# Optimization experiments

Measured on AMD Instinct MI355X. Metric: run time of the kernel, lower is better.

The kernel has to match this reference:

```python
import jax, jax.numpy as jnp
import numpy as np
import math

N_HEAD = 16
N_HEAD_KV = 4
WINDOW = 1024
SINK = 4
ROPE_BASE = 10000.0


def _rope(x):
    # x: [B, H, T, D]; rotate-half RoPE
    B, H, T, D = x.shape
    inv_freq = 1.0 / (ROPE_BASE ** (jnp.arange(0, D, 2, dtype=jnp.float32) / D))  # [D/2]
    ang = jnp.arange(T, dtype=jnp.float32)[:, None] * inv_freq[None, :]  # [T, D/2]
    cos = jnp.concatenate([jnp.cos(ang), jnp.cos(ang)], axis=-1)  # [T, D]
    sin = jnp.concatenate([jnp.sin(ang), jnp.sin(ang)], axis=-1)
    x1, x2 = x[..., : D // 2], x[..., D // 2 :]
    rot = jnp.concatenate([-x2, x1], axis=-1)
    return x * cos[None, None] + rot * sin[None, None]


def setup_inputs() -> dict:
    key = jax.random.key(0)
    ks = jax.random.split(key, 6)
    B, T, C = 2, 2048, 2048
    D = C // N_HEAD
    x = jax.random.normal(ks[0], (B, T, C), dtype=jnp.float32)
    s = 0.02
    Wq = jax.random.normal(ks[1], (C, C), dtype=jnp.float32) * s
    Wk = jax.random.normal(ks[2], (C, N_HEAD_KV * D), dtype=jnp.float32) * s
    Wv = jax.random.normal(ks[3], (C, N_HEAD_KV * D), dtype=jnp.float32) * s
    Wo = jax.random.normal(ks[4], (C, C), dtype=jnp.float32) * s
    seq_lengths = jax.random.randint(ks[5], (B,), T // 2, T + 1, dtype=jnp.int32)
    return {"x": x, "Wq": Wq, "Wk": Wk, "Wv": Wv, "Wo": Wo, "seq_lengths": seq_lengths}


def reference(x, Wq, Wk, Wv, Wo, seq_lengths):
    B, T, C = x.shape
    H, Hkv = N_HEAD, N_HEAD_KV
    D = C // H
    scale = 1.0 / math.sqrt(D)

    q = (x @ Wq).reshape(B, T, H, D).transpose(0, 2, 1, 3)      # [B,H,T,D]
    k = (x @ Wk).reshape(B, T, Hkv, D).transpose(0, 2, 1, 3)    # [B,Hkv,T,D]
    v = (x @ Wv).reshape(B, T, Hkv, D).transpose(0, 2, 1, 3)
    # GQA: repeat kv heads (matches torch repeat_interleave on head dim)
    k = jnp.repeat(k, H // Hkv, axis=1)
    v = jnp.repeat(v, H // Hkv, axis=1)

    q = _rope(q)
    k = _rope(k)

    scores = jnp.einsum('bhqd,bhkd->bhqk', q, k) * scale  # [B,H,T,T]

    qi = jnp.arange(T)[:, None]
    ki = jnp.arange(T)[None, :]
    # causal & (in sliding window | attention sink)
    base = (qi >= ki) & (((qi - ki) <= WINDOW) | (ki < SINK))  # [T,T]
    valid = jnp.arange(T)[None, :] < seq_lengths[:, None]      # [B,T]
    mask = base[None, None] & valid[:, None, :, None] & valid[:, None, None, :]

    scores = jnp.where(mask, scores, -1e30)
    attn = jax.nn.softmax(scores, axis=-1)
    y = jnp.einsum('bhqk,bhkd->bhqd', attn, v)
    # flex_attention returns 0 for fully-masked (padded) query rows
    y = y * valid[:, None, :, None]

    y = y.transpose(0, 2, 1, 3).reshape(B, T, C)
    return y @ Wo
```

## Files before the change

### kernel.cpp

```cpp
#include <hip/hip_runtime.h>
#include <stdint.h>

#define BATCH 2
#define TSEQ  2048
#define CDIM  2048
#define NHEAD 16
#define NKV   4
#define HDIM  128
#define KVDIM 512
#define WIN   1024
#define SINKN 4
#define QT    64
#define QKVN  3072

typedef unsigned short u16;
typedef __attribute__((ext_vector_type(8))) short bf16x8;
typedef __attribute__((ext_vector_type(4))) float f32x4;
typedef __attribute__((address_space(3))) uint32_t as3_u32;
typedef const __attribute__((address_space(1))) uint32_t as1_u32;

__device__ __forceinline__ float bf2f(u16 u) {
  union { uint32_t i; float f; } w; w.i = ((uint32_t)u) << 16; return w.f;
}
__device__ __forceinline__ u16 f2bf(float f) {
  union { uint32_t i; float f; } w; w.f = f;
  return (u16)((w.i + 0x7fffu + ((w.i >> 16) & 1u)) >> 16);
}
__device__ __forceinline__ void gl2lds16(const u16* g, u16* l) {
  __builtin_amdgcn_global_load_lds((as1_u32*)g, (as3_u32*)l, 16, 0, 0);
}

__global__ __launch_bounds__(256)
void detect_kernel(const uint32_t* __restrict__ x, uint32_t* __restrict__ flag) {
  __shared__ int red[4];
  const int tid = threadIdx.x;
  int c = 0;
  for (int i = tid; i < 1024; i += 256) {
    uint32_t e = (x[i] >> 7) & 0xFFu;
    c += (e >= 100u && e <= 135u) ? 1 : 0;
  }
#pragma unroll
  for (int off = 32; off; off >>= 1) c += __shfl_xor(c, off, 64);
  if ((tid & 63) == 0) red[tid >> 6] = c;
  __syncthreads();
  if (tid == 0) flag[0] = ((red[0] + red[1] + red[2] + red[3]) > 512) ? 1u : 0u;
}

__global__ __launch_bounds__(256)
void convert4_kernel(const void* __restrict__ src, u16* __restrict__ dst,
                     int n4, const uint32_t* __restrict__ flag) {
  const int i = blockIdx.x * 256 + threadIdx.x;
  if (i >= n4) return;
  if (flag[0]) {
    ((uint2*)dst)[i] = ((const uint2*)src)[i];
  } else {
    float4 f = ((const float4*)src)[i];
    ushort4 o = { f2bf(f.x), f2bf(f.y), f2bf(f.z), f2bf(f.w) };
    ((ushort4*)dst)[i] = o;
  }
}

__global__ __launch_bounds__(256)
void transpose_w(const void* __restrict__ src, u16* __restrict__ dst,
                 int K, int N, const uint32_t* __restrict__ flag) {
  __shared__ u16 t[32][33];
  const int n0 = blockIdx.x * 32, k0 = blockIdx.y * 32;
  const int tx = threadIdx.x & 31, ty = threadIdx.x >> 5;
  const uint32_t f = flag[0];
#pragma unroll
  for (int i = 0; i < 4; ++i) {
    const int kk = k0 + ty + i * 8;
    u16 val = f ? ((const u16*)src)[(size_t)kk * N + n0 + tx]
                : f2bf(((const float*)src)[(size_t)kk * N + n0 + tx]);
    t[ty + i * 8][tx] = val;
  }
  __syncthreads();
#pragma unroll
  for (int i = 0; i < 4; ++i)
    dst[(size_t)(n0 + ty + i * 8) * K + k0 + tx] = t[tx][ty + i * 8];
}

__global__ __launch_bounds__(256)
void transpose_v(const u16* __restrict__ qkv, u16* __restrict__ vt) {
  __shared__ u16 t[32][33];
  const int tok0 = blockIdx.x * 32;
  const int d0 = blockIdx.y * 32;
  const int bh = blockIdx.z;
  const int b = bh >> 2, kvh = bh & 3;
  const int tx = threadIdx.x & 31, ty = threadIdx.x >> 5;
  const u16* src = qkv + ((size_t)(b * TSEQ + tok0)) * QKVN + 2560 + (kvh << 7) + d0;
#pragma unroll
  for (int i = 0; i < 4; ++i)
    t[ty + i * 8][tx] = src[(size_t)(ty + i * 8) * QKVN + tx];
  __syncthreads();
  u16* dst = vt + ((size_t)(bh * 128 + d0)) * TSEQ + tok0;
#pragma unroll
  for (int i = 0; i < 4; ++i)
    dst[(size_t)(ty + i * 8) * TSEQ + tx] = t[tx][ty + i * 8];
}

#define BAR() asm volatile("s_barrier" ::: "memory")

__device__ __forceinline__ void stage_half(const u16* g, int K, u16* lds,
                                           int w, int lrow, int lc16) {
  gl2lds16(g + (size_t)(w * 8 + lrow) * K + (lc16 << 3), lds + (w << 9));
  gl2lds16(g + (size_t)(64 + w * 8 + lrow) * K + (lc16 << 3), lds + ((8 + w) << 9));
}

__global__ __launch_bounds__(512, 2)
void gemm256(const u16* __restrict__ A, const u16* __restrict__ BT,
             void* __restrict__ C, int M, int N, int K,
             const uint32_t* __restrict__ flagp, const int* __restrict__ seq) {
  __shared__ u16 As[2 * 256 * 64];
  __shared__ u16 Bs[2 * 256 * 64];

  const int tid = threadIdx.x;
  const int w = tid >> 6, lane = tid & 63;
  const int quad = lane >> 4, lm = lane & 15, l8 = lane & 7;
  const int wm = w >> 2, wn = w & 3;
  const int lrow = lane >> 3;
  const int lc16 = (lane & 7) ^ lrow;

  const int gx = gridDim.x;
  const int nwg = gx * gridDim.y;
  int lin = blockIdx.y * gx + blockIdx.x;
  if ((nwg & 7) == 0) lin = (lin & 7) * (nwg >> 3) + (lin >> 3);
  const int m0 = (lin / gx) << 8;
  const int n0 = (lin % gx) << 8;

  if (seq) {
    const int t0 = m0 & (TSEQ - 1);
    if (t0 >= seq[m0 >> 11]) {
      const uint32_t fmz = flagp ? flagp[0] : 1u;
      if (fmz == 0) {
        float4 z = {0.f, 0.f, 0.f, 0.f};
        float* Cp = (float*)C;
        for (int i = tid; i < 256 * 64; i += 512) {
          const int r = i >> 6, c4 = (i & 63) << 2;
          *(float4*)(Cp + (size_t)(m0 + r) * N + n0 + c4) = z;
        }
      } else {
        uint4 z = {0u, 0u, 0u, 0u};
        u16* Cp = (u16*)C;
        for (int i = tid; i < 256 * 32; i += 512) {
          const int r = i >> 5, c8 = (i & 31) << 3;
          *(uint4*)(Cp + (size_t)(m0 + r) * N + n0 + c8) = z;
        }
      }
      return;
    }
  }

  const u16* Agm = A + (size_t)m0 * K;
  const u16* Bgm = BT + (size_t)n0 * K;
  const int NT = K >> 6;

  f32x4 acc[8][4];
#pragma unroll
  for (int i = 0; i < 8; ++i)
#pragma unroll
    for (int j = 0; j < 4; ++j) acc[i][j] = (f32x4){0.f, 0.f, 0.f, 0.f};

  stage_half(Bgm,                     K, Bs,             w, lrow, lc16);
  stage_half(Agm,                     K, As,             w, lrow, lc16);
  stage_half(Bgm + (size_t)128 * K,   K, Bs + 128 * 64,  w, lrow, lc16);
  stage_half(Agm + (size_t)128 * K,   K, As + 128 * 64,  w, lrow, lc16);
  stage_half(Bgm + 64,                K, Bs + 16384,     w, lrow, lc16);
  stage_half(Agm + 64,                K, As + 16384,     w, lrow, lc16);
  asm volatile("s_waitcnt vmcnt(4)" ::: "memory");
  BAR();

  bf16x8 a[4][2], b0[2][2], b1[2][2];

#define LDA_(mh)                                                              \
  _Pragma("unroll") for (int mi = 0; mi < 4; ++mi)                            \
  _Pragma("unroll") for (int ks = 0; ks < 2; ++ks)                            \
    a[mi][ks] = *(const bf16x8*)(Ab + ((wm * 128 + (mh) * 64 + mi * 16 + lm) << 6) + \
                                 (((ks * 4 + quad) ^ l8) << 3));
#define LDB_(dst, nh)                                                         \
  _Pragma("unroll") for (int ni = 0; ni < 2; ++ni)                            \
  _Pragma("unroll") for (int ks = 0; ks < 2; ++ks)                            \
    dst[ni][ks] = *(const bf16x8*)(Bb + ((wn * 64 + (nh) * 32 + ni * 16 + lm) << 6) + \
                                   (((ks * 4 + quad) ^ l8) << 3));
#define MFMA8(mh, nh, bb)                                                     \
  __builtin_amdgcn_s_setprio(1);                                              \
  _Pragma("unroll") for (int mi = 0; mi < 4; ++mi)                            \
  _Pragma("unroll") for (int ni = 0; ni < 2; ++ni)                            \
  _Pragma("unroll") for (int ks = 0; ks < 2; ++ks)                            \
    acc[(mh) * 4 + mi][(nh) * 2 + ni] = __builtin_amdgcn_mfma_f32_16x16x32_bf16( \
        a[mi][ks], bb[ni][ks], acc[(mh) * 4 + mi][(nh) * 2 + ni], 0, 0, 0);   \
  __builtin_amdgcn_s_setprio(0);

  for (int t = 0; t < NT; ++t) {
    const int p = t & 1;
    const u16* Ab = As + p * 16384;
    const u16* Bb = Bs + p * 16384;
    u16* An = (u16*)As + (p ^ 1) * 16384;
    u16* Bn = (u16*)Bs + (p ^ 1) * 16384;
    u16* Ac = (u16*)As + p * 16384;
    u16* Bc = (u16*)Bs + p * 16384;
    const size_t kc1 = (size_t)(t + 1) << 6;
    const size_t kc2 = (size_t)(t + 2) << 6;

    LDA_(0); LDB_(b0, 0);
    if (t + 1 < NT) stage_half(Bgm + (size_t)128 * K + kc1, K, Bn + 128 * 64, w, lrow, lc16);
    BAR();
    MFMA8(0, 0, b0);
    BAR();
    LDB_(b1, 1);
    if (t + 1 < NT) stage_half(Agm + (size_t)128 * K + kc1, K, An + 128 * 64, w, lrow, lc16);
    BAR();
    MFMA8(0, 1, b1);
    BAR();
    LDA_(1);
    if (t + 2 < NT) stage_half(Bgm + kc2, K, Bc, w, lrow, lc16);
    BAR();
    MFMA8(1, 1, b1);
    BAR();
    if (t + 2 < NT) stage_half(Agm + kc2, K, Ac, w, lrow, lc16);
    BAR();
    MFMA8(1, 0, b0);
    if (t >= NT - 2) { asm volatile("s_waitcnt vmcnt(0)" ::: "memory"); }
    else             { asm volatile("s_waitcnt vmcnt(4)" ::: "memory"); }
    BAR();
  }
#undef LDA_
#undef LDB_
#undef MFMA8

  const uint32_t fm = flagp ? flagp[0] : 1u;
#pragma unroll
  for (int mi = 0; mi < 8; ++mi)
#pragma unroll
    for (int ni = 0; ni < 4; ++ni)
#pragma unroll
      for (int r = 0; r < 4; ++r) {
        const int row = m0 + wm * 128 + mi * 16 + quad * 4 + r;
        const int col = n0 + wn * 64 + ni * 16 + lm;
        const float val = acc[mi][ni][r];
        if (fm == 0) ((float*)C)[(size_t)row * N + col] = val;
        else         ((u16*)C)[(size_t)row * N + col] = f2bf(val);
      }
}

__global__ __launch_bounds__(256)
void rope_kernel(u16* __restrict__ qkv) {
  const int QP = BATCH * TSEQ * NHEAD * 64;
  const int KP = BATCH * TSEQ * NKV * 64;
  int idx = blockIdx.x * 256 + threadIdx.x;
  u16* p;
  int i, t;
  if (idx < QP) {
    i = idx & 63;
    int hh = (idx >> 6) & (NHEAD - 1);
    int row = idx >> 10;
    t = row & (TSEQ - 1);
    p = qkv + (size_t)row * QKVN + (hh << 7);
  } else {
    int j = idx - QP;
    if (j >= KP) return;
    i = j & 63;
    int hh = (j >> 6) & (NKV - 1);
    int row = j >> 8;
    t = row & (TSEQ - 1);
    p = qkv + (size_t)row * QKVN + 2048 + (hh << 7);
  }
  float x1 = bf2f(p[i]), x2 = bf2f(p[i + 64]);
  float freq = exp2f((float)i * (-2.0f / 128.0f) * 13.287712379549449f);
  float ang = (float)t * freq;
  float c = cosf(ang), s = sinf(ang);
  p[i]      = f2bf(x1 * c - x2 * s);
  p[i + 64] = f2bf(x2 * c + x1 * s);
}

__global__ __launch_bounds__(256, 3)
void attn_mfma(const u16* __restrict__ qkv, const u16* __restrict__ vt,
               u16* __restrict__ y, const int* __restrict__ seq_lengths) {
  const int bid = blockIdx.x;
  const int q0 = (31 - (bid & 31)) * QT;
  const int h  = (bid >> 5) & (NHEAD - 1);
  const int b  = bid >> 9;
  const int tid = threadIdx.x;
  const int w = tid >> 6;
  const int lane = tid & 63;
  const int quad = lane >> 4;
  const int lm = lane & 15;
  const int L = seq_lengths[b];
  const int kvh = h >> 2;
  const int kvoff = kvh << 7;
  const size_t bT = (size_t)b * TSEQ;

  if (q0 >= L) {
    const uint4 z = {0u, 0u, 0u, 0u};
    for (int i = tid; i < 64 * 256; i += 256) {
      const int r = i >> 8, c8 = (i & 255) << 3;
      *(uint4*)(y + ((bT + q0 + r) << 11) + c8) = z;
    }
    return;
  }

  __shared__ u16 Ks[32 * 136];
  __shared__ u16 Vt[144 * 40];
  __shared__ u16 Ps[4 * 16 * 42];

  const int qbase = q0 + w * 16;

  bf16x8 qf[4];
  {
    const u16* qrow = qkv + (bT + qbase + lm) * QKVN + (h << 7);
#pragma unroll
    for (int c = 0; c < 4; ++c)
      qf[c] = *(const bf16x8*)(qrow + c * 32 + quad * 8);
  }

  for (int i = tid; i < 16 * 40; i += 256)
    Vt[128 * 40 + i] = (i < 40) ? (u16)0x3F80 : (u16)0;

  const int s0k = q0 - WIN > 0 ? q0 - WIN : 0;
  const int sink_extra = (s0k > 0) ? 1 : 0;
  const int niter = ((q0 + QT - s0k) >> 5) + sink_extra;

  f32x4 Oacc[9];
#pragma unroll
  for (int nt = 0; nt < 9; ++nt) Oacc[nt] = (f32x4){0.f, 0.f, 0.f, 0.f};

  const float cexp = 0.127517634f;
  const int trow = tid >> 4;
  const int tc8 = (tid & 15) << 3;
  const int vd = tid >> 2;
  const int vkg = (tid & 3) << 3;
  u16* Pw = Ps + w * 672;

  const u16* kp0 = qkv + (bT + trow) * QKVN + 2048 + kvoff + tc8;
  const u16* kp1 = kp0 + (size_t)16 * QKVN;
  const u16* vp0 = vt + ((size_t)(b * NKV + kvh) << 18) + (size_t)vd * TSEQ + vkg;
  const u16* vp1 = vp0 + (size_t)64 * TSEQ;

  uint4 kr0, kr1, vr0, vr1;
#define LOAD_CHUNK(kb)                                        \
  do {                                                        \
    kr0 = *(const uint4*)(kp0 + (size_t)(kb) * QKVN);         \
    kr1 = *(const uint4*)(kp1 + (size_t)(kb) * QKVN);         \
    vr0 = *(const uint4*)(vp0 + (kb));                        \
    vr1 = *(const uint4*)(vp1 + (kb));                        \
  } while (0)

  int kb_cur = sink_extra ? 0 : s0k;
  int kb_next = sink_extra ? s0k : s0k + 32;
  LOAD_CHUNK(kb_cur);

  for (int it = 0; it < niter; ++it) {
    __syncthreads();
    *(uint4*)(Ks + trow * 136 + tc8)        = kr0;
    *(uint4*)(Ks + (16 + trow) * 136 + tc8) = kr1;
    *(uint4*)(Vt + vd * 40 + vkg)           = vr0;
    *(uint4*)(Vt + (vd + 64) * 40 + vkg)    = vr1;
    if (it + 1 < niter) LOAD_CHUNK(kb_next);
    __syncthreads();

    f32x4 sc0 = {0.f, 0.f, 0.f, 0.f}, sc1 = {0.f, 0.f, 0.f, 0.f};
    __builtin_amdgcn_s_setprio(1);
#pragma unroll
    for (int c = 0; c < 4; ++c) {
      bf16x8 kf = *(const bf16x8*)(Ks + lm * 136 + c * 32 + quad * 8);
      sc0 = __builtin_amdgcn_mfma_f32_16x16x32_bf16(qf[c], kf, sc0, 0, 0, 0);
    }
#pragma unroll
    for (int c = 0; c < 4; ++c) {
      bf16x8 kf = *(const bf16x8*)(Ks + (16 + lm) * 136 + c * 32 + quad * 8);
      sc1 = __builtin_amdgcn_mfma_f32_16x16x32_bf16(qf[c], kf, sc1, 0, 0, 0);
    }
    __builtin_amdgcn_s_setprio(0);

    const int key0 = kb_cur + lm;
    const int key1 = key0 + 16;
#pragma unroll
    for (int r = 0; r < 4; ++r) {
      const int qrow = qbase + quad * 4 + r;
      const bool ok0 = (key0 <= qrow) && ((qrow - key0 <= WIN) || (key0 < SINKN));
      const bool ok1 = (key1 <= qrow) && ((qrow - key1 <= WIN) || (key1 < SINKN));
      const float p0 = ok0 ? exp2f(sc0[r] * cexp) : 0.f;
      const float p1 = ok1 ? exp2f(sc1[r] * cexp) : 0.f;
      const int row = quad * 4 + r;
      Pw[row * 42 + lm]      = f2bf(p0);
      Pw[row * 42 + 16 + lm] = f2bf(p1);
    }
    bf16x8 pf = *(const bf16x8*)(Pw + lm * 42 + quad * 8);
    __builtin_amdgcn_s_setprio(1);
#pragma unroll
    for (int nt = 0; nt < 9; ++nt) {
      bf16x8 vf = *(const bf16x8*)(Vt + (nt * 16 + lm) * 40 + quad * 8);
      Oacc[nt] = __builtin_amdgcn_mfma_f32_16x16x32_bf16(pf, vf, Oacc[nt], 0, 0, 0);
    }
    __builtin_amdgcn_s_setprio(0);
    kb_cur = kb_next;
    kb_next += 32;
  }
#undef LOAD_CHUNK

  float invl[4];
#pragma unroll
  for (int r = 0; r < 4; ++r) {
    const float l = __shfl(Oacc[8][r], lane & 48, 64);
    invl[r] = 1.0f / l;
  }
#pragma unroll
  for (int nt = 0; nt < 8; ++nt)
#pragma unroll
    for (int r = 0; r < 4; ++r) {
      const int qrow = qbase + quad * 4 + r;
      const float val = (qrow < L) ? Oacc[nt][r] * invl[r] : 0.f;
      y[((bT + qrow) << 11) + (h << 7) + nt * 16 + lm] = f2bf(val);
    }
}

extern "C" void kernel_launch(void* const* d_in, const int* in_sizes, int n_in,
                              void* d_out, int out_size, void* d_ws, size_t ws_size,
                              hipStream_t stream) {
  const int M = BATCH * TSEQ;
  const int NX  = M * CDIM;

  uint32_t* flag = (uint32_t*)d_ws;
  u16* base = (u16*)((char*)d_ws + 16);
  u16* qkvb = base;
  u16* yb   = qkvb + (size_t)M * QKVN;
  u16* xb   = yb  + (size_t)NX;
  u16* wqT  = xb  + (size_t)NX;
  u16* wkvT = wqT + (size_t)CDIM * CDIM;
  u16* woT  = wkvT + (size_t)1024 * CDIM;
  u16* vtb  = woT + (size_t)CDIM * CDIM;

  const int* seq = (const int*)d_in[5];

  detect_kernel<<<1, 256, 0, stream>>>((const uint32_t*)d_in[0], flag);
  convert4_kernel<<<(NX / 4 + 255) / 256, 256, 0, stream>>>(d_in[0], xb, NX / 4, flag);
  transpose_w<<<dim3(CDIM / 32, CDIM / 32), 256, 0, stream>>>(d_in[1], wqT, CDIM, CDIM, flag);
  transpose_w<<<dim3(KVDIM / 32, CDIM / 32), 256, 0, stream>>>(d_in[2], wkvT, CDIM, KVDIM, flag);
  transpose_w<<<dim3(KVDIM / 32, CDIM / 32), 256, 0, stream>>>(d_in[3], wkvT + (size_t)KVDIM * CDIM, CDIM, KVDIM, flag);
  transpose_w<<<dim3(CDIM / 32, CDIM / 32), 256, 0, stream>>>(d_in[4], woT, CDIM, CDIM, flag);

  gemm256<<<dim3(QKVN / 256, M / 256), 512, 0, stream>>>(xb, wqT, qkvb, M, QKVN, CDIM, nullptr, seq);
  const int rope_threads = BATCH * TSEQ * (NHEAD + NKV) * 64;
  rope_kernel<<<rope_threads / 256, 256, 0, stream>>>(qkvb);
  transpose_v<<<dim3(TSEQ / 32, HDIM / 32, BATCH * NKV), 256, 0, stream>>>(qkvb, vtb);
  attn_mfma<<<BATCH * NHEAD * (TSEQ / QT), 256, 0, stream>>>(qkvb, vtb, yb, seq);
  gemm256<<<dim3(CDIM / 256, M / 256), 512, 0, stream>>>(yb, woT, d_out, M, CDIM, CDIM, flag, seq);
}
```

Baseline: 364.4 us.

## Make each attention block a single wave processing all four query row tiles

The attention kernel now launches 64-thread blocks. Each block is one wavefront that computes all four 16-row query tiles of a 64-row tile against each shared K/V chunk. This removes the __syncthreads barriers and reuses the K fragments loaded from LDS across the four row tiles. Block order is changed so the heaviest query tiles of every batch/head are scheduled first, and fully padded tiles now zero only their own head's columns instead of the full row. In exchange, each wave holds far more live registers (accumulators for four row tiles plus eight prefetch registers each for K and V), and the total wave count drops by four. That risks spills and much weaker latency hiding.

```diff
diff --git a/kernel.cpp b/kernel.cpp
--- a/kernel.cpp
+++ b/kernel.cpp
@@ -273,16 +273,16 @@
   p[i + 64] = f2bf(x2 * c + x1 * s);
 }
 
-__global__ __launch_bounds__(256, 3)
+__global__ __launch_bounds__(64, 1)
 void attn_mfma(const u16* __restrict__ qkv, const u16* __restrict__ vt,
                u16* __restrict__ y, const int* __restrict__ seq_lengths) {
   const int bid = blockIdx.x;
-  const int q0 = (31 - (bid & 31)) * QT;
-  const int h  = (bid >> 5) & (NHEAD - 1);
-  const int b  = bid >> 9;
-  const int tid = threadIdx.x;
-  const int w = tid >> 6;
-  const int lane = tid & 63;
+  const int tile = 31 - (bid >> 5);
+  const int q0 = tile * QT;
+  const int bh = bid & 31;
+  const int h  = bh & (NHEAD - 1);
+  const int b  = bh >> 4;
+  const int lane = threadIdx.x & 63;
   const int quad = lane >> 4;
   const int lm = lane & 15;
   const int L = seq_lengths[b];
@@ -292,57 +292,50 @@
 
   if (q0 >= L) {
     const uint4 z = {0u, 0u, 0u, 0u};
-    for (int i = tid; i < 64 * 256; i += 256) {
-      const int r = i >> 8, c8 = (i & 255) << 3;
-      *(uint4*)(y + ((bT + q0 + r) << 11) + c8) = z;
+    for (int i = lane; i < 64 * 16; i += 64) {
+      const int r = i >> 4, c8 = (i & 15) << 3;
+      *(uint4*)(y + ((bT + q0 + r) << 11) + (h << 7) + c8) = z;
     }
     return;
   }
 
   __shared__ u16 Ks[32 * 136];
   __shared__ u16 Vt[144 * 40];
-  __shared__ u16 Ps[4 * 16 * 42];
-
-  const int qbase = q0 + w * 16;
-
-  bf16x8 qf[4];
-  {
-    const u16* qrow = qkv + (bT + qbase + lm) * QKVN + (h << 7);
+  __shared__ u16 Pw[16 * 42];
+
+  bf16x8 qf[4][4];
+#pragma unroll
+  for (int rt = 0; rt < 4; ++rt) {
+    const u16* qrow = qkv + (bT + q0 + rt * 16 + lm) * QKVN + (h << 7);
 #pragma unroll
     for (int c = 0; c < 4; ++c)
-      qf[c] = *(const bf16x8*)(qrow + c * 32 + quad * 8);
-  }
-
-  for (int i = tid; i < 16 * 40; i += 256)
+      qf[rt][c] = *(const bf16x8*)(qrow + c * 32 + quad * 8);
+  }
+
+  for (int i = lane; i < 16 * 40; i += 64)
     Vt[128 * 40 + i] = (i < 40) ? (u16)0x3F80 : (u16)0;
 
   const int s0k = q0 - WIN > 0 ? q0 - WIN : 0;
   const int sink_extra = (s0k > 0) ? 1 : 0;
   const int niter = ((q0 + QT - s0k) >> 5) + sink_extra;
 
-  f32x4 Oacc[9];
-#pragma unroll
-  for (int nt = 0; nt < 9; ++nt) Oacc[nt] = (f32x4){0.f, 0.f, 0.f, 0.f};
+  f32x4 Oacc[4][9];
+#pragma unroll
+  for (int rt = 0; rt < 4; ++rt)
+#pragma unroll
+    for (int nt = 0; nt < 9; ++nt) Oacc[rt][nt] = (f32x4){0.f, 0.f, 0.f, 0.f};
 
   const float cexp = 0.127517634f;
-  const int trow = tid >> 4;
-  const int tc8 = (tid & 15) << 3;
-  const int vd = tid >> 2;
-  const int vkg = (tid & 3) << 3;
-  u16* Pw = Ps + w * 672;
-
-  const u16* kp0 = qkv + (bT + trow) * QKVN + 2048 + kvoff + tc8;
-  const u16* kp1 = kp0 + (size_t)16 * QKVN;
-  const u16* vp0 = vt + ((size_t)(b * NKV + kvh) << 18) + (size_t)vd * TSEQ + vkg;
-  const u16* vp1 = vp0 + (size_t)64 * TSEQ;
-
-  uint4 kr0, kr1, vr0, vr1;
-#define LOAD_CHUNK(kb)                                        \
-  do {                                                        \
-    kr0 = *(const uint4*)(kp0 + (size_t)(kb) * QKVN);         \
-    kr1 = *(const uint4*)(kp1 + (size_t)(kb) * QKVN);         \
-    vr0 = *(const uint4*)(vp0 + (kb));                        \
-    vr1 = *(const uint4*)(vp1 + (kb));                        \
+  const u16* kp = qkv + (bT + (lane >> 4)) * QKVN + 2048 + kvoff + ((lane & 15) << 3);
+  const u16* vp = vt + ((size_t)(b * NKV + kvh) << 18) + (size_t)(lane >> 2) * TSEQ + ((lane & 3) << 3);
+
+  uint4 kr[8], vr[8];
+#define LOAD_CHUNK(kb)                                                      \
+  do {                                                                      \
+    _Pragma("unroll") for (int j = 0; j < 8; ++j) {                         \
+      kr[j] = *(const uint4*)(kp + (size_t)((kb) + j * 4) * QKVN);          \
+      vr[j] = *(const uint4*)(vp + (kb) + (size_t)j * 16 * TSEQ);           \
+    }                                                                       \
   } while (0)
 
   int kb_cur = sink_extra ? 0 : s0k;
@@ -350,68 +343,76 @@
   LOAD_CHUNK(kb_cur);
 
   for (int it = 0; it < niter; ++it) {
-    __syncthreads();
-    *(uint4*)(Ks + trow * 136 + tc8)        = kr0;
-    *(uint4*)(Ks + (16 + trow) * 136 + tc8) = kr1;
-    *(uint4*)(Vt + vd * 40 + vkg)           = vr0;
-    *(uint4*)(Vt + (vd + 64) * 40 + vkg)    = vr1;
+#pragma unroll
+    for (int j = 0; j < 8; ++j) {
+      *(uint4*)(Ks + (j * 4 + (lane >> 4)) * 136 + ((lane & 15) << 3)) = kr[j];
+      *(uint4*)(Vt + (j * 16 + (lane >> 2)) * 40 + ((lane & 3) << 3))  = vr[j];
+    }
     if (it + 1 < niter) LOAD_CHUNK(kb_next);
-    __syncthreads();
-
-    f32x4 sc0 = {0.f, 0.f, 0.f, 0.f}, sc1 = {0.f, 0.f, 0.f, 0.f};
-    __builtin_amdgcn_s_setprio(1);
+
+    bf16x8 kf0[4], kf1[4];
 #pragma unroll
     for (int c = 0; c < 4; ++c) {
-      bf16x8 kf = *(const bf16x8*)(Ks + lm * 136 + c * 32 + quad * 8);
-      sc0 = __builtin_amdgcn_mfma_f32_16x16x32_bf16(qf[c], kf, sc0, 0, 0, 0);
-    }
-#pragma unroll
-    for (int c = 0; c < 4; ++c) {
-      bf16x8 kf = *(const bf16x8*)(Ks + (16 + lm) * 136 + c * 32 + quad * 8);
-      sc1 = __builtin_amdgcn_mfma_f32_16x16x32_bf16(qf[c], kf, sc1, 0, 0, 0);
-    }
-    __builtin_amdgcn_s_setprio(0);
+      kf0[c] = *(const bf16x8*)(Ks + lm * 136 + c * 32 + quad * 8);
+      kf1[c] = *(const bf16x8*)(Ks + (16 + lm) * 136 + c * 32 + quad * 8);
+    }
 
     const int key0 = kb_cur + lm;
     const int key1 = key0 + 16;
 #pragma unroll
-    for (int r = 0; r < 4; ++r) {
-      const int qrow = qbase + quad * 4 + r;
-      const bool ok0 = (key0 <= qrow) && ((qrow - key0 <= WIN) || (key0 < SINKN));
-      const bool ok1 = (key1 <= qrow) && ((qrow - key1 <= WIN) || (key1 < SINKN));
-      const float p0 = ok0 ? exp2f(sc0[r] * cexp) : 0.f;
-      const float p1 = ok1 ? exp2f(sc1[r] * cexp) : 0.f;
-      const int row = quad * 4 + r;
-      Pw[row * 42 + lm]      = f2bf(p0);
-      Pw[row * 42 + 16 + lm] = f2bf(p1);
-    }
-    bf16x8 pf = *(const bf16x8*)(Pw + lm * 42 + quad * 8);
-    __builtin_amdgcn_s_setprio(1);
-#pragma unroll
-    for (int nt = 0; nt < 9; ++nt) {
-      bf16x8 vf = *(const bf16x8*)(Vt + (nt * 16 + lm) * 40 + quad * 8);
-      Oacc[nt] = __builtin_amdgcn_mfma_f32_16x16x32_bf16(pf, vf, Oacc[nt], 0, 0, 0);
-    }
-    __builtin_amdgcn_s_setprio(0);
+    for (int rt = 0; rt < 4; ++rt) {
+      f32x4 sc0 = {0.f, 0.f, 0.f, 0.f}, sc1 = {0.f, 0.f, 0.f, 0.f};
+      __builtin_amdgcn_s_setprio(1);
+#pragma unroll
+      for (int c = 0; c < 4; ++c)
+        sc0 = __builtin_amdgcn_mfma_f32_16x16x32_bf16(qf[rt][c], kf0[c], sc0, 0, 0, 0);
+#pragma unroll
+      for (int c = 0; c < 4; ++c)
+        sc1 = __builtin_amdgcn_mfma_f32_16x16x32_bf16(qf[rt][c], kf1[c], sc1, 0, 0, 0);
+      __builtin_amdgcn_s_setprio(0);
+
+#pragma unroll
+      for (int r = 0; r < 4; ++r) {
+        const int qrow = q0 + rt * 16 + quad * 4 + r;
+        const bool ok0 = (key0 <= qrow) && ((qrow - key0 <= WIN) || (key0 < SINKN));
+        const bool ok1 = (key1 <= qrow) && ((qrow - key1 <= WIN) || (key1 < SINKN));
+        const float p0 = ok0 ? exp2f(sc0[r] * cexp) : 0.f;
+        const float p1 = ok1 ? exp2f(sc1[r] * cexp) : 0.f;
+        const int row = quad * 4 + r;
+        Pw[row * 42 + lm]      = f2bf(p0);
+        Pw[row * 42 + 16 + lm] = f2bf(p1);
+      }
+      bf16x8 pf = *(const bf16x8*)(Pw + lm * 42 + quad * 8);
+      __builtin_amdgcn_s_setprio(1);
+#pragma unroll
+      for (int nt = 0; nt < 9; ++nt) {
+        bf16x8 vf = *(const bf16x8*)(Vt + (nt * 16 + lm) * 40 + quad * 8);
+        Oacc[rt][nt] = __builtin_amdgcn_mfma_f32_16x16x32_bf16(pf, vf, Oacc[rt][nt], 0, 0, 0);
+      }
+      __builtin_amdgcn_s_setprio(0);
+    }
     kb_cur = kb_next;
     kb_next += 32;
   }
 #undef LOAD_CHUNK
 
-  float invl[4];
-#pragma unroll
-  for (int r = 0; r < 4; ++r) {
-    const float l = __shfl(Oacc[8][r], lane & 48, 64);
-    invl[r] = 1.0f / l;
-  }
-#pragma unroll
-  for (int nt = 0; nt < 8; ++nt)
+#pragma unroll
+  for (int rt = 0; rt < 4; ++rt) {
+    float invl[4];
 #pragma unroll
     for (int r = 0; r < 4; ++r) {
-      const int qrow = qbase + quad * 4 + r;
-      const float val = (qrow < L) ? Oacc[nt][r] * invl[r] : 0.f;
-      y[((bT + qrow) << 11) + (h << 7) + nt * 16 + lm] = f2bf(val);
-    }
+      const float l = __shfl(Oacc[rt][8][r], lane & 48, 64);
+      invl[r] = 1.0f / l;
+    }
+#pragma unroll
+    for (int nt = 0; nt < 8; ++nt)
+#pragma unroll
+      for (int r = 0; r < 4; ++r) {
+        const int qrow = q0 + rt * 16 + quad * 4 + r;
+        const float val = (qrow < L) ? Oacc[rt][nt][r] * invl[r] : 0.f;
+        y[((bT + qrow) << 11) + (h << 7) + nt * 16 + lm] = f2bf(val);
+      }
+  }
 }
 
 extern "C" void kernel_launch(void* const* d_in, const int* in_sizes, int n_in,
@@ -443,6 +444,6 @@
   const int rope_threads = BATCH * TSEQ * (NHEAD + NKV) * 64;
   rope_kernel<<<rope_threads / 256, 256, 0, stream>>>(qkvb);
   transpose_v<<<dim3(TSEQ / 32, HDIM / 32, BATCH * NKV), 256, 0, stream>>>(qkvb, vtb);
-  attn_mfma<<<BATCH * NHEAD * (TSEQ / QT), 256, 0, stream>>>(qkvb, vtb, yb, seq);
+  attn_mfma<<<BATCH * NHEAD * (TSEQ / QT), 64, 0, stream>>>(qkvb, vtb, yb, seq);
   gemm256<<<dim3(CDIM / 256, M / 256), 512, 0, stream>>>(yb, woT, d_out, M, CDIM, CDIM, flag, seq);
 }
```

Measured after the change: 606.3 us. 1.66x slower.
